# Performance work log

Hardware: AMD Instinct MI355X
Metric: run time of the kernel (lower is better)

## Reference

```python
import jax, jax.numpy as jnp
import numpy as np

B, N, E, H = 4, 1024, 1024, 16
D = E // H

def setup_inputs() -> dict:
    key = jax.random.key(0)
    ks = jax.random.split(key, 5)
    return {
        "x": jax.random.normal(ks[0], (B, N, E), dtype=jnp.float32),
        "Wqkv": jax.random.normal(ks[1], (E, 3 * E), dtype=jnp.float32) * 0.02,
        "bqkv": jax.random.normal(ks[2], (3 * E,), dtype=jnp.float32) * 0.02,
        "Wfc": jax.random.normal(ks[3], (E, E), dtype=jnp.float32) * 0.02,
        "bfc": jax.random.normal(ks[4], (E,), dtype=jnp.float32) * 0.02,
    }

def reference(x, Wqkv, bqkv, Wfc, bfc):
    b, n, e = x.shape
    h, d = H, E // H
    qkv = x @ Wqkv + bqkv                      # [b, n, 3e]
    q, k, v = jnp.split(qkv, 3, axis=-1)       # each [b, n, e]
    # view to [b, n, h, d] then RAW reshape to [b, h, n, d] (faithful to original,
    # which uses .reshape, not transpose — mixes seq/head axes)
    q = q.reshape(b, n, h, d).reshape(b, h, n, d)
    k = k.reshape(b, n, h, d).reshape(b, h, n, d)
    v = v.reshape(b, n, h, d).reshape(b, h, n, d)
    scores = jnp.einsum('bhqd,bhkd->bhqk', q, k) / jnp.sqrt(jnp.float32(d))
    causal = jnp.triu(jnp.ones((n, n), dtype=bool), k=1)  # True above diagonal
    scores = jnp.where(causal, -jnp.inf, scores)
    attn = jax.nn.softmax(scores, axis=-1)
    out = jnp.einsum('bhqk,bhkd->bhqd', attn, v)          # [b, h, n, d]
    # raw reshape back to [b, n, h, d] then flatten heads (faithful)
    out = out.reshape(b, n, h, d).reshape(b, n, e)
    return out @ Wfc + bfc
```

## Files before the change

kernel.cpp:

```cpp
#include <hip/hip_runtime.h>


typedef __bf16 bf16x8 __attribute__((ext_vector_type(8)));
typedef float f32x4 __attribute__((ext_vector_type(4)));

#define QSCALE 0.18033688011112042f
#define DEFER_THR 11.0f

__device__ __forceinline__ unsigned short f2bf(float f) {
    unsigned u = __float_as_uint(f);
    u += 0x7fffu + ((u >> 16) & 1u);
    return (unsigned short)(u >> 16);
}

__device__ __forceinline__ unsigned cvtpk_bf16(float lo, float hi) {
    unsigned r;
    asm("v_cvt_pk_bf16_f32 %0, %1, %2" : "=v"(r) : "v"(lo), "v"(hi));
    return r;
}

union FragU { uint4 u; bf16x8 v; };

__device__ __forceinline__ bf16x8 ld_frag(const unsigned short* p) {
    FragU x; x.u = *(const uint4*)p; return x.v;
}

__device__ __forceinline__ void gload_lds16(const void* g, void* l) {
    __builtin_amdgcn_global_load_lds(
        (const __attribute__((address_space(1))) void*)g,
        (__attribute__((address_space(3))) void*)l, 16, 0, 0);
}

__global__ __launch_bounds__(256) void prep(
    const float* __restrict__ x,    unsigned short* __restrict__ xb,
    const float* __restrict__ Wqkv, unsigned short* __restrict__ wqkvT,
    const float* __restrict__ Wfc,  unsigned short* __restrict__ wfcT)
{
    __shared__ float tile[32][33];
    int bid = blockIdx.x;
    int tx = threadIdx.x & 31, ty = threadIdx.x >> 5;
    if (bid < 3072) {
        int c0 = (bid % 96) * 32, r0 = (bid / 96) * 32;
        for (int i = ty; i < 32; i += 8)
            tile[i][tx] = Wqkv[(r0 + i) * 3072 + c0 + tx];
        __syncthreads();
        for (int i = ty; i < 32; i += 8)
            wqkvT[(long)(c0 + i) * 1024 + r0 + tx] = f2bf(tile[tx][i]);
    } else if (bid < 4096) {
        int b2 = bid - 3072;
        int c0 = (b2 % 32) * 32, r0 = (b2 / 32) * 32;
        for (int i = ty; i < 32; i += 8)
            tile[i][tx] = Wfc[(r0 + i) * 1024 + c0 + tx];
        __syncthreads();
        for (int i = ty; i < 32; i += 8)
            wfcT[(long)(c0 + i) * 1024 + r0 + tx] = f2bf(tile[tx][i]);
    } else {
        const int n4 = 1 << 20;
        for (int i = (bid - 4096) * 256 + threadIdx.x; i < n4; i += 1024 * 256) {
            float4 f = ((const float4*)x)[i];
            unsigned a = (unsigned)f2bf(f.x) | ((unsigned)f2bf(f.y) << 16);
            unsigned b = (unsigned)f2bf(f.z) | ((unsigned)f2bf(f.w) << 16);
            ((uint2*)xb)[i] = make_uint2(a, b);
        }
    }
}

__global__ void transpose_v(const unsigned short* __restrict__ v,
                            unsigned short* __restrict__ vt) {
    __shared__ unsigned short tile[32][33];
    int bh = blockIdx.z;
    int n0 = blockIdx.x * 32, d0 = blockIdx.y * 32;
    const unsigned short* src = v + (long)bh * 65536;
    unsigned short* dst = vt + (long)bh * 65536;
    for (int i = threadIdx.y; i < 32; i += 8)
        tile[i][threadIdx.x] = src[(n0 + i) * 64 + d0 + threadIdx.x];
    __syncthreads();
    for (int i = threadIdx.y; i < 32; i += 8)
        dst[(d0 + i) * 1024 + n0 + threadIdx.x] = tile[threadIdx.x][i];
}

template <int MODE>
__global__ __launch_bounds__(256) void gemm128(
    const unsigned short* __restrict__ A,
    const unsigned short* __restrict__ Bt,
    const float* __restrict__ bias,
    unsigned short* __restrict__ qb,
    unsigned short* __restrict__ kb,
    unsigned short* __restrict__ vb,
    float* __restrict__ outf)
{
    const int K = 1024;
    __shared__ unsigned short As[2][4096];
    __shared__ unsigned short Bs[2][4096];
    int t = threadIdx.x, lane = t & 63, w = t >> 6;
    int wm = w >> 1, wn = w & 1;
    int lrow = lane >> 4, lcol = lane & 15;

    const int NX  = (MODE == 0) ? 24 : 8;
    const int CPX = (MODE == 0) ? 96 : 32;
    int id = blockIdx.x;
    int idp = (id & 7) * CPX + (id >> 3);
    int tn0 = (idp % NX) * 128, tm0 = (idp / NX) * 128;

    int seg0 = w * 1024;
    int seg1 = (w + 4) * 1024;
    int off0 = seg0 + lane * 16, off1 = seg1 + lane * 16;
    int r0 = off0 >> 6, cb0 = off0 & 63;
    int r1 = off1 >> 6, cb1 = off1 & 63;

    const char* gA = (const char*)A;
    const char* gB = (const char*)Bt;

    f32x4 acc[4][4] = {};

    auto STAGE = [&](int buf, int kt) {
        long kby = (long)kt * 2;
        gload_lds16(gA + (long)(tm0 + r0) * 2048 + kby + cb0, (char*)&As[buf][0] + seg0);
        gload_lds16(gA + (long)(tm0 + r1) * 2048 + kby + cb1, (char*)&As[buf][0] + seg1);
        gload_lds16(gB + (long)(tn0 + r0) * 2048 + kby + cb0, (char*)&Bs[buf][0] + seg0);
        gload_lds16(gB + (long)(tn0 + r1) * 2048 + kby + cb1, (char*)&Bs[buf][0] + seg1);
    };

    STAGE(0, 0);
    asm volatile("s_waitcnt vmcnt(0)");
    __syncthreads();

    int cur = 0;
    for (int kt = 0; kt < K; kt += 32) {
        if (kt + 32 < K) STAGE(cur ^ 1, kt + 32);

        bf16x8 af[4], bfr[4];
        #pragma unroll
        for (int mi = 0; mi < 4; ++mi)
            af[mi] = ld_frag(&As[cur][0] + (wm * 64 + mi * 16 + lcol) * 32 + lrow * 8);
        #pragma unroll
        for (int ni = 0; ni < 4; ++ni)
            bfr[ni] = ld_frag(&Bs[cur][0] + (wn * 64 + ni * 16 + lcol) * 32 + lrow * 8);
        #pragma unroll
        for (int mi = 0; mi < 4; ++mi)
            #pragma unroll
            for (int ni = 0; ni < 4; ++ni)
                acc[mi][ni] = __builtin_amdgcn_mfma_f32_16x16x32_bf16(af[mi], bfr[ni], acc[mi][ni], 0, 0, 0);

        __syncthreads();
        cur ^= 1;
    }

    #pragma unroll
    for (int mi = 0; mi < 4; ++mi) {
        int gr0 = tm0 + wm * 64 + mi * 16 + lrow * 4;
        #pragma unroll
        for (int ni = 0; ni < 4; ++ni) {
            int gc = tn0 + wn * 64 + ni * 16 + lcol;
            float bv = bias[gc];
            if (MODE == 0) {
                int sec = gc >> 10, ei = gc & 1023;
                unsigned short* dst = sec == 0 ? qb : (sec == 1 ? kb : vb);
                if (sec == 0) {
                    #pragma unroll
                    for (int r = 0; r < 4; ++r)
                        dst[(long)(gr0 + r) * 1024 + ei] = f2bf((acc[mi][ni][r] + bv) * QSCALE);
                } else {
                    #pragma unroll
                    for (int r = 0; r < 4; ++r)
                        dst[(long)(gr0 + r) * 1024 + ei] = f2bf(acc[mi][ni][r] + bv);
                }
            } else {
                #pragma unroll
                for (int r = 0; r < 4; ++r)
                    outf[(long)(gr0 + r) * 1024 + gc] = acc[mi][ni][r] + bv;
            }
        }
    }
}

__global__ __launch_bounds__(256) void attn(
    const unsigned short* __restrict__ qbuf,
    const unsigned short* __restrict__ kbuf,
    const unsigned short* __restrict__ vtbuf,
    unsigned short* __restrict__ obuf)
{
    __shared__ char smem[17920] __attribute__((aligned(16)));
    unsigned short (*Ps)[32][40] = (unsigned short (*)[32][40])smem;
    _Float16* accH = (_Float16*)smem;
    float* mS = (float*)(smem + 17408);

    int id = blockIdx.x;
    int xcd = id & 7, slot = id >> 3;
    int bh = xcd + 8 * (slot >> 4);
    int j = slot & 15;

    const unsigned short* Q  = qbuf + (long)bh * 65536;
    const unsigned short* Kp = kbuf + (long)bh * 65536;
    const unsigned short* VT = vtbuf + (long)bh * 65536;
    unsigned short* O = obuf + (long)bh * 65536;
    int t = threadIdx.x, lane = t & 63, w = t >> 6;
    int lrow = lane >> 4, lcol = lane & 15;
    const float NEG = -__builtin_inff();

    #pragma unroll
    for (int pass = 0; pass < 2; ++pass) {
        int qt = pass == 0 ? j : 31 - j;
        int qbase = qt * 32;
        int T = qt + 1;

        bf16x8 qf[2][2];
        #pragma unroll
        for (int qg = 0; qg < 2; ++qg)
            #pragma unroll
            for (int kc = 0; kc < 2; ++kc)
                qf[qg][kc] = ld_frag(Q + (long)(qbase + qg * 16 + lcol) * 64 + kc * 32 + lrow * 8);

        f32x4 acc[2][4] = {};
        float m_i[2] = {NEG, NEG};
        float lsum[2][2] = {{0.f, 0.f}, {0.f, 0.f}};

        if (w < T) {
            int kt = w * 32;
            bf16x8 kf[2][2];
            #pragma unroll
            for (int kg = 0; kg < 2; ++kg)
                #pragma unroll
                for (int kc = 0; kc < 2; ++kc)
                    kf[kg][kc] = ld_frag(Kp + (long)(kt + kg * 16 + lcol) * 64 + kc * 32 + lrow * 8);

            for (;;) {
                f32x4 s[2][2] = {};
                __builtin_amdgcn_s_setprio(1);
                #pragma unroll
                for (int kg = 0; kg < 2; ++kg)
                    #pragma unroll
                    for (int kc = 0; kc < 2; ++kc) {
                        s[0][kg] = __builtin_amdgcn_mfma_f32_16x16x32_bf16(kf[kg][kc], qf[0][kc], s[0][kg], 0, 0, 0);
                        s[1][kg] = __builtin_amdgcn_mfma_f32_16x16x32_bf16(kf[kg][kc], qf[1][kc], s[1][kg], 0, 0, 0);
                    }
                __builtin_amdgcn_s_setprio(0);

                int ktn = kt + 128;
                bool more = ktn < T * 32;
                if (more) {
                    #pragma unroll
                    for (int kg = 0; kg < 2; ++kg)
                        #pragma unroll
                        for (int kc = 0; kc < 2; ++kc)
                            kf[kg][kc] = ld_frag(Kp + (long)(ktn + kg * 16 + lcol) * 64 + kc * 32 + lrow * 8);
                }
                bf16x8 vf[4];
                #pragma unroll
                for (int dg = 0; dg < 4; ++dg)
                    vf[dg] = ld_frag(VT + (long)(dg * 16 + lcol) * 1024 + kt + lrow * 8);

                float tv[2][8], lmax[2];
                bool diag = (kt == qbase);
                #pragma unroll
                for (int qg = 0; qg < 2; ++qg) {
                    #pragma unroll
                    for (int kg = 0; kg < 2; ++kg)
                        #pragma unroll
                        for (int r = 0; r < 4; ++r)
                            tv[qg][kg * 4 + r] = s[qg][kg][r];
                    if (diag) {
                        #pragma unroll
                        for (int kg = 0; kg < 2; ++kg)
                            #pragma unroll
                            for (int r = 0; r < 4; ++r)
                                if (kg * 16 + lrow * 4 + r > qg * 16 + lcol)
                                    tv[qg][kg * 4 + r] = NEG;
                    }
                    float a0 = fmaxf(tv[qg][0], tv[qg][1]), a1 = fmaxf(tv[qg][2], tv[qg][3]);
                    float a2 = fmaxf(tv[qg][4], tv[qg][5]), a3 = fmaxf(tv[qg][6], tv[qg][7]);
                    lmax[qg] = fmaxf(fmaxf(a0, a1), fmaxf(a2, a3));
                }

                bool ok = (lmax[0] <= m_i[0] + DEFER_THR) && (lmax[1] <= m_i[1] + DEFER_THR);
                if (!__all(ok)) {
                    #pragma unroll
                    for (int qg = 0; qg < 2; ++qg) {
                        float mx = fmaxf(lmax[qg], __shfl_xor(lmax[qg], 16));
                        mx = fmaxf(mx, __shfl_xor(mx, 32));
                        float mnew = fmaxf(m_i[qg], mx);
                        float alpha = exp2f(m_i[qg] - mnew);
                        m_i[qg] = mnew;
                        lsum[qg][0] *= alpha;
                        lsum[qg][1] *= alpha;
                        #pragma unroll
                        for (int dg = 0; dg < 4; ++dg)
                            #pragma unroll
                            for (int r = 0; r < 4; ++r)
                                acc[qg][dg][r] *= alpha;
                    }
                }

                #pragma unroll
                for (int qg = 0; qg < 2; ++qg) {
                    float p[8];
                    #pragma unroll
                    for (int jj = 0; jj < 8; ++jj) p[jj] = exp2f(tv[qg][jj] - m_i[qg]);
                    lsum[qg][0] += (p[0] + p[1]) + (p[2] + p[3]);
                    lsum[qg][1] += (p[4] + p[5]) + (p[6] + p[7]);
                    unsigned u0 = cvtpk_bf16(p[0], p[1]);
                    unsigned u1 = cvtpk_bf16(p[2], p[3]);
                    unsigned u2 = cvtpk_bf16(p[4], p[5]);
                    unsigned u3 = cvtpk_bf16(p[6], p[7]);
                    *(uint2*)&Ps[w][qg * 16 + lcol][lrow * 4]      = make_uint2(u0, u1);
                    *(uint2*)&Ps[w][qg * 16 + lcol][16 + lrow * 4] = make_uint2(u2, u3);
                }

                bf16x8 pb[2];
                pb[0] = ld_frag(&Ps[w][lcol][lrow * 8]);
                pb[1] = ld_frag(&Ps[w][16 + lcol][lrow * 8]);
                __builtin_amdgcn_s_setprio(1);
                #pragma unroll
                for (int dg = 0; dg < 4; ++dg) {
                    acc[0][dg] = __builtin_amdgcn_mfma_f32_16x16x32_bf16(vf[dg], pb[0], acc[0][dg], 0, 0, 0);
                    acc[1][dg] = __builtin_amdgcn_mfma_f32_16x16x32_bf16(vf[dg], pb[1], acc[1][dg], 0, 0, 0);
                }
                __builtin_amdgcn_s_setprio(0);

                if (!more) break;
                kt = ktn;
            }
        }

        __syncthreads();
        #pragma unroll
        for (int qg = 0; qg < 2; ++qg) {
            int q = qg * 16 + lcol;
            float lr = lsum[qg][0] + lsum[qg][1];
            lr += __shfl_xor(lr, 16);
            lr += __shfl_xor(lr, 32);
            float mprime, inv;
            if (lr > 0.f) { mprime = m_i[qg] + log2f(lr); inv = 1.f / lr; }
            else          { mprime = NEG; inv = 0.f; }
            if (lrow == 0) mS[w * 32 + q] = mprime;
            #pragma unroll
            for (int dg = 0; dg < 4; ++dg) {
                _Float16 a0 = (_Float16)(acc[qg][dg][0] * inv);
                _Float16 a1 = (_Float16)(acc[qg][dg][1] * inv);
                _Float16 a2 = (_Float16)(acc[qg][dg][2] * inv);
                _Float16 a3 = (_Float16)(acc[qg][dg][3] * inv);
                _Float16* dst = &accH[(w * 32 + q) * 68 + dg * 16 + lrow * 4];
                dst[0] = a0; dst[1] = a1; dst[2] = a2; dst[3] = a3;
            }
        }
        __syncthreads();

        {
            int qq = t >> 3, d0 = (t & 7) * 8;
            float m0 = mS[qq], m1 = mS[32 + qq], m2 = mS[64 + qq], m3 = mS[96 + qq];
            float M = fmaxf(fmaxf(m0, m1), fmaxf(m2, m3));
            float e0 = exp2f(m0 - M), e1 = exp2f(m1 - M), e2 = exp2f(m2 - M), e3 = exp2f(m3 - M);
            float inv = 1.f / (e0 + e1 + e2 + e3);
            const _Float16* a0 = &accH[qq * 68 + d0];
            const _Float16* a1 = &accH[(32 + qq) * 68 + d0];
            const _Float16* a2 = &accH[(64 + qq) * 68 + d0];
            const _Float16* a3 = &accH[(96 + qq) * 68 + d0];
            unsigned short h[8];
            #pragma unroll
            for (int jj = 0; jj < 8; ++jj)
                h[jj] = f2bf((e0 * (float)a0[jj] + e1 * (float)a1[jj] +
                              e2 * (float)a2[jj] + e3 * (float)a3[jj]) * inv);
            uint4 pk;
            pk.x = (unsigned)h[0] | ((unsigned)h[1] << 16);
            pk.y = (unsigned)h[2] | ((unsigned)h[3] << 16);
            pk.z = (unsigned)h[4] | ((unsigned)h[5] << 16);
            pk.w = (unsigned)h[6] | ((unsigned)h[7] << 16);
            *(uint4*)&O[(long)(qbase + qq) * 64 + d0] = pk;
        }
        __syncthreads();
    }
}

extern "C" void kernel_launch(void* const* d_in, const int* in_sizes, int n_in,
                              void* d_out, int out_size, void* d_ws, size_t ws_size,
                              hipStream_t stream) {
    const float* x    = (const float*)d_in[0];
    const float* Wqkv = (const float*)d_in[1];
    const float* bqkv = (const float*)d_in[2];
    const float* Wfc  = (const float*)d_in[3];
    const float* bfc  = (const float*)d_in[4];
    float* out = (float*)d_out;

    unsigned short* ws    = (unsigned short*)d_ws;
    unsigned short* xb    = ws;
    unsigned short* wqkvT = xb + (4u << 20);
    unsigned short* wfcT  = wqkvT + (3u << 20);
    unsigned short* qb    = wfcT + (1u << 20);
    unsigned short* kb    = qb + (4u << 20);
    unsigned short* vb    = kb + (4u << 20);
    unsigned short* vbT   = xb;
    unsigned short* ob    = vb;

    prep<<<dim3(5120), dim3(256), 0, stream>>>(x, xb, Wqkv, wqkvT, Wfc, wfcT);
    gemm128<0><<<dim3(768), dim3(256), 0, stream>>>(xb, wqkvT, bqkv, qb, kb, vb, nullptr);
    transpose_v<<<dim3(32, 2, 64), dim3(32, 8), 0, stream>>>(vb, vbT);
    attn<<<dim3(1024), dim3(256), 0, stream>>>(qb, kb, vbT, ob);
    gemm128<1><<<dim3(256), dim3(256), 0, stream>>>(ob, wfcT, bfc, nullptr, nullptr, nullptr, out);
}
```

Measured before the change: 116.2 us.

## Restructure attention to stage shared K/V tiles in LDS across four query waves

The attention kernel changes from split-K-per-wave, where four waves share one 32-row query tile and merge partial softmax through LDS, to one 128-query block per launch with each wave owning 32 queries. K and V tiles are streamed into LDS with double-buffered async global-to-LDS loads and an XOR swizzle, so all four waves reuse them. This removes the cross-wave merge and the redundant per-wave global fragment loads. Blocks are ordered so the longest causal rows run first. The costs are intra-block load imbalance (lower waves skip many key tiles), barriers every tile, and half as many blocks.

New measurement: 111.4 us. -4.1%, faster.

```diff
diff --git a/kernel.cpp b/kernel.cpp
--- a/kernel.cpp
+++ b/kernel.cpp
@@ -180,51 +180,76 @@
     const unsigned short* __restrict__ vtbuf,
     unsigned short* __restrict__ obuf)
 {
-    __shared__ char smem[17920] __attribute__((aligned(16)));
-    unsigned short (*Ps)[32][40] = (unsigned short (*)[32][40])smem;
-    _Float16* accH = (_Float16*)smem;
-    float* mS = (float*)(smem + 17408);
+    __shared__ unsigned short Ks[2][4096];
+    __shared__ unsigned short Vs[2][4096];
+    __shared__ unsigned short Ps[4][32][40];
 
     int id = blockIdx.x;
-    int xcd = id & 7, slot = id >> 3;
-    int bh = xcd + 8 * (slot >> 4);
-    int j = slot & 15;
-
-    const unsigned short* Q  = qbuf + (long)bh * 65536;
-    const unsigned short* Kp = kbuf + (long)bh * 65536;
-    const unsigned short* VT = vtbuf + (long)bh * 65536;
+    int xcd = id & 7, s_ = id >> 3;
+    int j  = 7 - (s_ >> 3);
+    int bh = xcd + 8 * (s_ & 7);
+
+    const char* Kb = (const char*)(kbuf + (long)bh * 65536);
+    const char* Vb = (const char*)(vtbuf + (long)bh * 65536);
+    const unsigned short* Q = qbuf + (long)bh * 65536;
     unsigned short* O = obuf + (long)bh * 65536;
+
     int t = threadIdx.x, lane = t & 63, w = t >> 6;
     int lrow = lane >> 4, lcol = lane & 15;
     const float NEG = -__builtin_inff();
 
+    int qbase = j * 128 + w * 32;
+    int T = 2 * j + 2;
+
+    int row0 = w * 8 + (lane >> 3);
+    int slot = (((lane & 7) ^ (lane >> 3)) << 4);
+
+    auto STAGE = [&](int buf, int kt) {
+        long k2 = (long)kt * 2;
+        gload_lds16(Kb + (k2 + row0 * 2) * 64 + slot,        (char*)&Ks[buf][0] + w * 1024);
+        gload_lds16(Kb + (k2 + (row0 + 32) * 2) * 64 + slot, (char*)&Ks[buf][0] + 4096 + w * 1024);
+        gload_lds16(Vb + (long)row0 * 2048 + k2 + slot,        (char*)&Vs[buf][0] + w * 1024);
+        gload_lds16(Vb + (long)(row0 + 32) * 2048 + k2 + slot, (char*)&Vs[buf][0] + 4096 + w * 1024);
+    };
+
+    bf16x8 qf[2][2];
     #pragma unroll
-    for (int pass = 0; pass < 2; ++pass) {
-        int qt = pass == 0 ? j : 31 - j;
-        int qbase = qt * 32;
-        int T = qt + 1;
-
-        bf16x8 qf[2][2];
-        #pragma unroll
-        for (int qg = 0; qg < 2; ++qg)
-            #pragma unroll
-            for (int kc = 0; kc < 2; ++kc)
-                qf[qg][kc] = ld_frag(Q + (long)(qbase + qg * 16 + lcol) * 64 + kc * 32 + lrow * 8);
-
-        f32x4 acc[2][4] = {};
-        float m_i[2] = {NEG, NEG};
-        float lsum[2][2] = {{0.f, 0.f}, {0.f, 0.f}};
-
-        if (w < T) {
-            int kt = w * 32;
-            bf16x8 kf[2][2];
-            #pragma unroll
-            for (int kg = 0; kg < 2; ++kg)
-                #pragma unroll
-                for (int kc = 0; kc < 2; ++kc)
-                    kf[kg][kc] = ld_frag(Kp + (long)(kt + kg * 16 + lcol) * 64 + kc * 32 + lrow * 8);
-
-            for (;;) {
+    for (int qg = 0; qg < 2; ++qg)
+        #pragma unroll
+        for (int kc = 0; kc < 2; ++kc)
+            qf[qg][kc] = ld_frag(Q + (long)(qbase + qg * 16 + lcol) * 64 + kc * 32 + lrow * 8);
+
+    f32x4 acc[2][4] = {};
+    float m_i[2] = {NEG, NEG};
+    float lsum[2][2] = {{0.f, 0.f}, {0.f, 0.f}};
+
+    STAGE(0, 0);
+    STAGE(1, 64);
+
+    for (int tt = 0; tt < T; ++tt) {
+        if (tt + 1 < T) asm volatile("s_waitcnt vmcnt(4)" ::: "memory");
+        else            asm volatile("s_waitcnt vmcnt(0)" ::: "memory");
+        __builtin_amdgcn_s_barrier();
+
+        int cur = tt & 1;
+        #pragma unroll
+        for (int ks = 0; ks < 2; ++ks) {
+            int kt_sub = tt * 64 + ks * 32;
+            if (kt_sub <= qbase) {
+                bf16x8 kf[2][2], vf[4];
+                #pragma unroll
+                for (int kg = 0; kg < 2; ++kg)
+                    #pragma unroll
+                    for (int kc = 0; kc < 2; ++kc) {
+                        int row = ks * 32 + kg * 16 + lcol;
+                        kf[kg][kc] = ld_frag(&Ks[cur][row * 64 + (((kc * 4 + lrow) ^ (row & 7)) << 3)]);
+                    }
+                #pragma unroll
+                for (int dg = 0; dg < 4; ++dg) {
+                    int row = dg * 16 + lcol;
+                    vf[dg] = ld_frag(&Vs[cur][row * 64 + (((ks * 4 + lrow) ^ (row & 7)) << 3)]);
+                }
+
                 f32x4 s[2][2] = {};
                 __builtin_amdgcn_s_setprio(1);
                 #pragma unroll
@@ -236,42 +261,24 @@
                     }
                 __builtin_amdgcn_s_setprio(0);
 
-                int ktn = kt + 128;
-                bool more = ktn < T * 32;
-                if (more) {
-                    #pragma unroll
-                    for (int kg = 0; kg < 2; ++kg)
-                        #pragma unroll
-                        for (int kc = 0; kc < 2; ++kc)
-                            kf[kg][kc] = ld_frag(Kp + (long)(ktn + kg * 16 + lcol) * 64 + kc * 32 + lrow * 8);
-                }
-                bf16x8 vf[4];
-                #pragma unroll
-                for (int dg = 0; dg < 4; ++dg)
-                    vf[dg] = ld_frag(VT + (long)(dg * 16 + lcol) * 1024 + kt + lrow * 8);
-
-                float tv[2][8], lmax[2];
-                bool diag = (kt == qbase);
-                #pragma unroll
-                for (int qg = 0; qg < 2; ++qg) {
-                    #pragma unroll
-                    for (int kg = 0; kg < 2; ++kg)
-                        #pragma unroll
-                        for (int r = 0; r < 4; ++r)
-                            tv[qg][kg * 4 + r] = s[qg][kg][r];
-                    if (diag) {
+                bool diag = (kt_sub == qbase);
+                if (diag) {
+                    #pragma unroll
+                    for (int qg = 0; qg < 2; ++qg)
                         #pragma unroll
                         for (int kg = 0; kg < 2; ++kg)
                             #pragma unroll
                             for (int r = 0; r < 4; ++r)
                                 if (kg * 16 + lrow * 4 + r > qg * 16 + lcol)
-                                    tv[qg][kg * 4 + r] = NEG;
-                    }
-                    float a0 = fmaxf(tv[qg][0], tv[qg][1]), a1 = fmaxf(tv[qg][2], tv[qg][3]);
-                    float a2 = fmaxf(tv[qg][4], tv[qg][5]), a3 = fmaxf(tv[qg][6], tv[qg][7]);
+                                    s[qg][kg][r] = NEG;
+                }
+                float lmax[2];
+                #pragma unroll
+                for (int qg = 0; qg < 2; ++qg) {
+                    float a0 = fmaxf(s[qg][0][0], s[qg][0][1]), a1 = fmaxf(s[qg][0][2], s[qg][0][3]);
+                    float a2 = fmaxf(s[qg][1][0], s[qg][1][1]), a3 = fmaxf(s[qg][1][2], s[qg][1][3]);
                     lmax[qg] = fmaxf(fmaxf(a0, a1), fmaxf(a2, a3));
                 }
-
                 bool ok = (lmax[0] <= m_i[0] + DEFER_THR) && (lmax[1] <= m_i[1] + DEFER_THR);
                 if (!__all(ok)) {
                     #pragma unroll
@@ -290,12 +297,14 @@
                                 acc[qg][dg][r] *= alpha;
                     }
                 }
-
                 #pragma unroll
                 for (int qg = 0; qg < 2; ++qg) {
                     float p[8];
                     #pragma unroll
-                    for (int jj = 0; jj < 8; ++jj) p[jj] = exp2f(tv[qg][jj] - m_i[qg]);
+                    for (int kg = 0; kg < 2; ++kg)
+                        #pragma unroll
+                        for (int r = 0; r < 4; ++r)
+                            p[kg * 4 + r] = exp2f(s[qg][kg][r] - m_i[qg]);
                     lsum[qg][0] += (p[0] + p[1]) + (p[2] + p[3]);
                     lsum[qg][1] += (p[4] + p[5]) + (p[6] + p[7]);
                     unsigned u0 = cvtpk_bf16(p[0], p[1]);
@@ -309,6 +318,7 @@
                 bf16x8 pb[2];
                 pb[0] = ld_frag(&Ps[w][lcol][lrow * 8]);
                 pb[1] = ld_frag(&Ps[w][16 + lcol][lrow * 8]);
+
                 __builtin_amdgcn_s_setprio(1);
                 #pragma unroll
                 for (int dg = 0; dg < 4; ++dg) {
@@ -316,58 +326,29 @@
                     acc[1][dg] = __builtin_amdgcn_mfma_f32_16x16x32_bf16(vf[dg], pb[1], acc[1][dg], 0, 0, 0);
                 }
                 __builtin_amdgcn_s_setprio(0);
-
-                if (!more) break;
-                kt = ktn;
             }
         }
 
-        __syncthreads();
-        #pragma unroll
-        for (int qg = 0; qg < 2; ++qg) {
-            int q = qg * 16 + lcol;
-            float lr = lsum[qg][0] + lsum[qg][1];
-            lr += __shfl_xor(lr, 16);
-            lr += __shfl_xor(lr, 32);
-            float mprime, inv;
-            if (lr > 0.f) { mprime = m_i[qg] + log2f(lr); inv = 1.f / lr; }
-            else          { mprime = NEG; inv = 0.f; }
-            if (lrow == 0) mS[w * 32 + q] = mprime;
-            #pragma unroll
-            for (int dg = 0; dg < 4; ++dg) {
-                _Float16 a0 = (_Float16)(acc[qg][dg][0] * inv);
-                _Float16 a1 = (_Float16)(acc[qg][dg][1] * inv);
-                _Float16 a2 = (_Float16)(acc[qg][dg][2] * inv);
-                _Float16 a3 = (_Float16)(acc[qg][dg][3] * inv);
-                _Float16* dst = &accH[(w * 32 + q) * 68 + dg * 16 + lrow * 4];
-                dst[0] = a0; dst[1] = a1; dst[2] = a2; dst[3] = a3;
-            }
+        __builtin_amdgcn_s_barrier();
+        if (tt + 2 < T) STAGE(cur, (tt + 2) * 64);
+    }
+
+    #pragma unroll
+    for (int qg = 0; qg < 2; ++qg) {
+        float lr = lsum[qg][0] + lsum[qg][1];
+        lr += __shfl_xor(lr, 16);
+        lr += __shfl_xor(lr, 32);
+        float inv = 1.f / lr;
+        int q = qbase + qg * 16 + lcol;
+        #pragma unroll
+        for (int dg = 0; dg < 4; ++dg) {
+            ushort4 pk;
+            pk.x = f2bf(acc[qg][dg][0] * inv);
+            pk.y = f2bf(acc[qg][dg][1] * inv);
+            pk.z = f2bf(acc[qg][dg][2] * inv);
+            pk.w = f2bf(acc[qg][dg][3] * inv);
+            *(ushort4*)&O[(long)q * 64 + dg * 16 + lrow * 4] = pk;
         }
-        __syncthreads();
-
-        {
-            int qq = t >> 3, d0 = (t & 7) * 8;
-            float m0 = mS[qq], m1 = mS[32 + qq], m2 = mS[64 + qq], m3 = mS[96 + qq];
-            float M = fmaxf(fmaxf(m0, m1), fmaxf(m2, m3));
-            float e0 = exp2f(m0 - M), e1 = exp2f(m1 - M), e2 = exp2f(m2 - M), e3 = exp2f(m3 - M);
-            float inv = 1.f / (e0 + e1 + e2 + e3);
-            const _Float16* a0 = &accH[qq * 68 + d0];
-            const _Float16* a1 = &accH[(32 + qq) * 68 + d0];
-            const _Float16* a2 = &accH[(64 + qq) * 68 + d0];
-            const _Float16* a3 = &accH[(96 + qq) * 68 + d0];
-            unsigned short h[8];
-            #pragma unroll
-            for (int jj = 0; jj < 8; ++jj)
-                h[jj] = f2bf((e0 * (float)a0[jj] + e1 * (float)a1[jj] +
-                              e2 * (float)a2[jj] + e3 * (float)a3[jj]) * inv);
-            uint4 pk;
-            pk.x = (unsigned)h[0] | ((unsigned)h[1] << 16);
-            pk.y = (unsigned)h[2] | ((unsigned)h[3] << 16);
-            pk.z = (unsigned)h[4] | ((unsigned)h[5] << 16);
-            pk.w = (unsigned)h[6] | ((unsigned)h[7] << 16);
-            *(uint4*)&O[(long)(qbase + qq) * 64 + d0] = pk;
-        }
-        __syncthreads();
     }
 }
 
@@ -394,6 +375,6 @@
     prep<<<dim3(5120), dim3(256), 0, stream>>>(x, xb, Wqkv, wqkvT, Wfc, wfcT);
     gemm128<0><<<dim3(768), dim3(256), 0, stream>>>(xb, wqkvT, bqkv, qb, kb, vb, nullptr);
     transpose_v<<<dim3(32, 2, 64), dim3(32, 8), 0, stream>>>(vb, vbT);
-    attn<<<dim3(1024), dim3(256), 0, stream>>>(qb, kb, vbT, ob);
+    attn<<<dim3(512), dim3(256), 0, stream>>>(qb, kb, vbT, ob);
     gemm128<1><<<dim3(256), dim3(256), 0, stream>>>(ob, wfcT, bfc, nullptr, nullptr, nullptr, out);
 }
```
